# Performance work log

Measured on AMD Instinct MI355X. Metric: run time of the kernel, lower is better.

The kernel has to match this reference:

```python
import jax, jax.numpy as jnp
import numpy as np

B, N, T, F = 16, 512, 24, 64


def setup_inputs() -> dict:
    key = jax.random.key(0)
    k1, k2, k3, k4 = jax.random.split(key, 4)
    ori_flow = jax.random.normal(k1, (B, N, T, F), dtype=jnp.float32)
    uncer = jax.random.normal(k2, (B, N, T, F), dtype=jnp.float32)
    spatial_embedding = jax.random.normal(k3, (N, F), dtype=jnp.float32)
    # nn.Linear(channels, channels, bias=False): y = x @ W.T, W: (out, in)
    W1 = jax.random.normal(k4, (F, F), dtype=jnp.float32) * (1.0 / np.sqrt(F))
    return {"ori_flow": ori_flow, "uncer": uncer,
            "spatial_embedding": spatial_embedding, "W1": W1}


def reference(ori_flow, uncer, spatial_embedding, W1):
    b, n, t, f = ori_flow.shape
    # (B, N, T, f) -> (B*T, N, f)
    x = ori_flow.transpose(0, 2, 1, 3).reshape(-1, n, f)
    u = uncer.transpose(0, 2, 1, 3).reshape(-1, n, f)
    # spatial embedding is identical across batch and time after expand/permute
    emb = jnp.broadcast_to(spatial_embedding, (b * t, n, f))
    h = jnp.concatenate([x, emb], axis=-1)            # (B*T, N, 2f)
    rel = jax.nn.relu(jnp.einsum('bnf,bmf->bnm', h, h))  # (B*T, N, N)
    rel = jax.nn.softmax(rel, axis=-1)                # dropout p=0 -> identity
    # sharing_paras=True: both branches use linear1 (no bias)
    of = jax.nn.relu(jnp.einsum('bnm,bmf->bnf', rel, x) @ W1.T)
    uf = jax.nn.relu(jnp.einsum('bnm,bmf->bnf', rel, u) @ W1.T)
    of = of.reshape(b, t, n, f).transpose(0, 2, 1, 3)  # (B, N, T, f)
    uf = uf.reshape(b, t, n, f).transpose(0, 2, 1, 3)
    return of, uf
```

## Files before the change

### kernel.cpp

```cpp
#include <hip/hip_runtime.h>
#include <hip/hip_bf16.h>

#define BB 16
#define NN 512
#define TT 24
#define FF 64
#define OUT_OFF ((size_t)BB*NN*TT*FF)

#define AIS 136
#define XTS 72
#define XTSZ 4672

typedef __attribute__((ext_vector_type(8))) short v8s;
typedef __attribute__((ext_vector_type(16))) float v16f;

union U16x8 { uint4 v; unsigned short s[8]; };

__device__ inline v16f mfma32(v8s a, v8s b, v16f c) {
    return __builtin_amdgcn_mfma_f32_32x32x16_bf16(a, b, c, 0, 0, 0);
}

__device__ inline unsigned int fbits(float x) {
    union { float f; unsigned int u; } c; c.f = x; return c.u;
}
__device__ inline float ibits(unsigned int u) {
    union { float f; unsigned int u; } c; c.u = u; return c.f;
}
__device__ inline unsigned short f2bf_r(float x) {
    return (unsigned short)((fbits(x) + 0x8000u) >> 16);
}
__device__ inline void split8(const float* f, U16x8& H, U16x8& L) {
    #pragma unroll
    for (int k = 0; k < 8; ++k) {
        unsigned int u  = fbits(f[k]);
        unsigned int hr = (u + 0x8000u) & 0xffff0000u;
        H.s[k] = (unsigned short)(hr >> 16);
        float lo = f[k] - ibits(hr);
        L.s[k] = (unsigned short)((fbits(lo) + 0x8000u) >> 16);
    }
}
__device__ inline void cvt8h(const float* f, U16x8& H) {
    #pragma unroll
    for (int k = 0; k < 8; ++k) H.s[k] = f2bf_r(f[k]);
}

__device__ inline unsigned int pkbf(float a, float b) {
    unsigned int r;
    asm("v_cvt_pk_bf16_f32 %0, %1, %2" : "=v"(r) : "v"(a), "v"(b));
    return r;
}

__device__ inline v8s pfrag(const float* cr, int c) {
    unsigned int a0 = pkbf(cr[8*c+0], cr[8*c+1]);
    unsigned int a1 = pkbf(cr[8*c+2], cr[8*c+3]);
    unsigned int b0 = pkbf(cr[8*c+4], cr[8*c+5]);
    unsigned int b1 = pkbf(cr[8*c+6], cr[8*c+7]);
    asm("v_permlane32_swap_b32 %0, %1" : "+v"(a0), "+v"(b0));
    asm("v_permlane32_swap_b32 %0, %1" : "+v"(a1), "+v"(b1));
    union { v8s v; unsigned int u[4]; } P;
    P.u[0] = a0; P.u[1] = a1; P.u[2] = b0; P.u[3] = b1;
    return P.v;
}

__global__ __launch_bounds__(256, 2)
void spag_kernel(const float* __restrict__ ori, const float* __restrict__ unc,
                 const float* __restrict__ emb, const float* __restrict__ W1,
                 float* __restrict__ out)
{
    __shared__ __align__(16) unsigned short SH[2*64*AIS + 2*XTSZ];
    unsigned short* AjH = SH;
    unsigned short* AjL = SH + 64*AIS;
    unsigned short* XT  = SH + 2*64*AIS;
    unsigned short* UT  = XT + XTSZ;

    const int tid  = threadIdx.x;
    const int xcd  = blockIdx.x & 7;
    const int slot = blockIdx.x >> 3;
    const int bt   = xcd * 48 + (slot >> 2);
    const int it   = slot & 3;
    const int b    = bt / TT, t = bt % TT;
    const int i0   = it * 128;

    const int lane = tid & 63;
    const int w    = tid >> 6;
    const int m    = lane & 31;
    const int hi   = lane >> 5;

    const int pj  = tid >> 3;
    const int f0  = (tid & 7) * 8;
    const int jme = 2 * pj;

    float pa0[8], pa1[8], pu0[8], pu1[8];
    {
        const size_t r0 = ((size_t)((b*NN + jme)*TT + t))*FF + f0;
        const size_t r1 = r0 + (size_t)TT*FF;
        *(float4*)&pa0[0] = *(const float4*)(ori + r0);
        *(float4*)&pa0[4] = *(const float4*)(ori + r0 + 4);
        *(float4*)&pa1[0] = *(const float4*)(ori + r1);
        *(float4*)&pa1[4] = *(const float4*)(ori + r1 + 4);
        *(float4*)&pu0[0] = *(const float4*)(unc + r0);
        *(float4*)&pu0[4] = *(const float4*)(unc + r0 + 4);
        *(float4*)&pu1[0] = *(const float4*)(unc + r1);
        *(float4*)&pu1[4] = *(const float4*)(unc + r1 + 4);
    }

    v8s bH[8], bL[8];
    #pragma unroll
    for (int p = 0; p < 2; ++p) {
        {
            const int sr = tid >> 2, fc = (tid & 3) * 16;
            const float* xb = ori + ((size_t)((b*NN + i0 + p*64 + sr)*TT + t))*FF + fc;
            const float* eb = emb + (size_t)(i0 + p*64 + sr)*FF + fc;
            float tf[8]; U16x8 H, L;
            #pragma unroll
            for (int h = 0; h < 2; ++h) {
                *(float4*)&tf[0] = ((const float4*)xb)[2*h];
                *(float4*)&tf[4] = ((const float4*)xb)[2*h+1];
                split8(tf, H, L);
                *(uint4*)&AjH[sr*AIS + fc + h*8] = H.v;
                *(uint4*)&AjL[sr*AIS + fc + h*8] = L.v;
                *(float4*)&tf[0] = ((const float4*)eb)[2*h];
                *(float4*)&tf[4] = ((const float4*)eb)[2*h+1];
                split8(tf, H, L);
                *(uint4*)&AjH[sr*AIS + 64 + fc + h*8] = H.v;
                *(uint4*)&AjL[sr*AIS + 64 + fc + h*8] = L.v;
            }
        }
        __syncthreads();
        if ((w >> 1) == p) {
            const int lr = (w & 1)*32 + m;
            #pragma unroll
            for (int kk = 0; kk < 8; ++kk) {
                bH[kk] = *(const v8s*)&AjH[lr*AIS + kk*16 + hi*8];
                bL[kk] = *(const v8s*)&AjL[lr*AIS + kk*16 + hi*8];
            }
        }
        __syncthreads();
    }

    v16f accX0 = (v16f)(0.0f), accX1 = (v16f)(0.0f);
    v16f accU0 = (v16f)(0.0f), accU1 = (v16f)(0.0f);
    float rs    = 0.0f;
    float m_run = 0.0f;

    for (int jt = 0; jt < 8; ++jt) {
        const int j0 = jt * 64;
        __syncthreads();

        {
            const int j = jme;
            U16x8 H0, L0, H1, L1;
            split8(pa0, H0, L0); split8(pa1, H1, L1);
            *(uint4*)&AjH[ j   *AIS + f0] = H0.v;
            *(uint4*)&AjH[(j+1)*AIS + f0] = H1.v;
            *(uint4*)&AjL[ j   *AIS + f0] = L0.v;
            *(uint4*)&AjL[(j+1)*AIS + f0] = L1.v;
            #pragma unroll
            for (int k = 0; k < 8; ++k) {
                int f = f0 + k;
                int off = f*XTS + (f>>4)*16 + j;
                *(unsigned int*)&XT[off] =
                    (unsigned int)H0.s[k] | ((unsigned int)H1.s[k] << 16);
            }
            #pragma unroll
            for (int k = 0; k < 8; ++k) {
                int f = f0 + k;
                int off = f*XTS + (f>>4)*16 + j;
                *(unsigned int*)&UT[off] =
                    (unsigned int)f2bf_r(pu0[k]) | ((unsigned int)f2bf_r(pu1[k]) << 16);
            }
            const float* e0 = emb + (size_t)(j0 + j)*FF + f0;
            float t0[8], t1[8];
            *(float4*)&t0[0] = *(const float4*)(e0);
            *(float4*)&t0[4] = *(const float4*)(e0 + 4);
            *(float4*)&t1[0] = *(const float4*)(e0 + FF);
            *(float4*)&t1[4] = *(const float4*)(e0 + FF + 4);
            split8(t0, H0, L0); split8(t1, H1, L1);
            *(uint4*)&AjH[ j   *AIS + 64 + f0] = H0.v;
            *(uint4*)&AjH[(j+1)*AIS + 64 + f0] = H1.v;
            *(uint4*)&AjL[ j   *AIS + 64 + f0] = L0.v;
            *(uint4*)&AjL[(j+1)*AIS + 64 + f0] = L1.v;
        }
        __syncthreads();

        if (jt < 7) {
            const size_t r0 = ((size_t)((b*NN + j0 + 64 + jme)*TT + t))*FF + f0;
            const size_t r1 = r0 + (size_t)TT*FF;
            *(float4*)&pa0[0] = *(const float4*)(ori + r0);
            *(float4*)&pa0[4] = *(const float4*)(ori + r0 + 4);
            *(float4*)&pa1[0] = *(const float4*)(ori + r1);
            *(float4*)&pa1[4] = *(const float4*)(ori + r1 + 4);
            *(float4*)&pu0[0] = *(const float4*)(unc + r0);
            *(float4*)&pu0[4] = *(const float4*)(unc + r0 + 4);
            *(float4*)&pu1[0] = *(const float4*)(unc + r1);
            *(float4*)&pu1[4] = *(const float4*)(unc + r1 + 4);
        }

        v16f C0 = (v16f)(0.0f), C1 = (v16f)(0.0f);
        #pragma unroll
        for (int kk = 0; kk < 8; ++kk) {
            const int fo = kk*16 + hi*8;
            v8s aH0 = *(const v8s*)&AjH[ m     *AIS + fo];
            v8s aL0 = *(const v8s*)&AjL[ m     *AIS + fo];
            v8s aH1 = *(const v8s*)&AjH[(32+m)*AIS + fo];
            v8s aL1 = *(const v8s*)&AjL[(32+m)*AIS + fo];
            C0 = mfma32(aH0, bH[kk], C0);
            C1 = mfma32(aH1, bH[kk], C1);
            C0 = mfma32(aH0, bL[kk], C0);
            C1 = mfma32(aH1, bL[kk], C1);
            C0 = mfma32(aL0, bH[kk], C0);
            C1 = mfma32(aL1, bH[kk], C1);
        }

        float mt = 0.0f;
        #pragma unroll
        for (int r = 0; r < 16; ++r) {
            float s0 = fmaxf(C0[r], 0.0f); C0[r] = s0;
            float s1 = fmaxf(C1[r], 0.0f); C1[r] = s1;
            mt = fmaxf(mt, fmaxf(s0, s1));
        }
        mt = fmaxf(mt, __shfl_xor(mt, 32));
        if (!__all(mt <= m_run + 8.0f)) {
            float m_new = fmaxf(m_run, mt);
            float al = __expf(m_run - m_new);
            rs *= al; m_run = m_new;
            #pragma unroll
            for (int r = 0; r < 16; ++r) {
                float a = __shfl(al, (r & 3) + 8*(r >> 2) + 4*hi);
                accX0[r] *= a; accX1[r] *= a;
                accU0[r] *= a; accU1[r] *= a;
            }
        }

        v8s P[4];
        {
            float cr[16];
            #pragma unroll
            for (int r = 0; r < 16; ++r) {
                float e = __expf(C0[r] - m_run);
                cr[r] = ibits((fbits(e) + 0x8000u) & 0xffff0000u);
                rs += cr[r];
            }
            P[0] = pfrag(cr, 0);
            P[1] = pfrag(cr, 1);
            #pragma unroll
            for (int r = 0; r < 16; ++r) {
                float e = __expf(C1[r] - m_run);
                cr[r] = ibits((fbits(e) + 0x8000u) & 0xffff0000u);
                rs += cr[r];
            }
            P[2] = pfrag(cr, 0);
            P[3] = pfrag(cr, 1);
        }

        #pragma unroll
        for (int kk = 0; kk < 4; ++kk) {
            const int fo = kk*16 + hi*8;
            v8s bx0 = *(const v8s*)&XT[ m     *XTS + (( m    )>>4)*16 + fo];
            v8s bu0 = *(const v8s*)&UT[ m     *XTS + (( m    )>>4)*16 + fo];
            v8s bx1 = *(const v8s*)&XT[(32+m)*XTS + (((32+m))>>4)*16 + fo];
            v8s bu1 = *(const v8s*)&UT[(32+m)*XTS + (((32+m))>>4)*16 + fo];
            accX0 = mfma32(P[kk], bx0, accX0);
            accX1 = mfma32(P[kk], bx1, accX1);
            accU0 = mfma32(P[kk], bu0, accU0);
            accU1 = mfma32(P[kk], bu1, accU1);
        }
    }

    __syncthreads();
    rs += __shfl_xor(rs, 32);
    float inv = 1.0f / rs;

    unsigned short* Ox = SH;
    unsigned short* Ou = SH + 128*XTS;
    unsigned short* Wt = SH + 256*XTS;

    #pragma unroll
    for (int r = 0; r < 16; ++r) {
        int il = (r & 3) + 8*(r >> 2) + 4*hi;
        float iv = __shfl(inv, il);
        int row = w*32 + il;
        Ox[row*XTS + m]      = f2bf_r(accX0[r] * iv);
        Ox[row*XTS + 32 + m] = f2bf_r(accX1[r] * iv);
        Ou[row*XTS + m]      = f2bf_r(accU0[r] * iv);
        Ou[row*XTS + 32 + m] = f2bf_r(accU1[r] * iv);
    }
    {
        const int sr = tid >> 2, fc = (tid & 3) * 16;
        const float* wb = W1 + sr*FF + fc;
        float tf[8]; U16x8 H;
        #pragma unroll
        for (int h = 0; h < 2; ++h) {
            *(float4*)&tf[0] = ((const float4*)wb)[2*h];
            *(float4*)&tf[4] = ((const float4*)wb)[2*h+1];
            cvt8h(tf, H);
            *(uint4*)&Wt[sr*XTS + fc + h*8] = H.v;
        }
    }
    __syncthreads();

    v8s ao[4], aq[4];
    #pragma unroll
    for (int kk = 0; kk < 4; ++kk) {
        const int fo = kk*16 + hi*8;
        ao[kk] = *(const v8s*)&Ox[(w*32 + m)*XTS + fo];
        aq[kk] = *(const v8s*)&Ou[(w*32 + m)*XTS + fo];
    }
    #pragma unroll
    for (int ot = 0; ot < 2; ++ot) {
        v16f ax = (v16f)(0.0f), au = (v16f)(0.0f);
        #pragma unroll
        for (int kk = 0; kk < 4; ++kk) {
            const int fo = kk*16 + hi*8;
            v8s bw = *(const v8s*)&Wt[(ot*32 + m)*XTS + fo];
            ax = mfma32(ao[kk], bw, ax);
            au = mfma32(aq[kk], bw, au);
        }
        #pragma unroll
        for (int r = 0; r < 16; ++r) {
            int il = (r & 3) + 8*(r >> 2) + 4*hi;
            int i = i0 + w*32 + il;
            int o = ot*32 + m;
            size_t idx = ((size_t)((b*NN + i)*TT + t))*FF + o;
            out[idx]           = fmaxf(ax[r], 0.0f);
            out[OUT_OFF + idx] = fmaxf(au[r], 0.0f);
        }
    }
}

extern "C" void kernel_launch(void* const* d_in, const int* in_sizes, int n_in,
                              void* d_out, int out_size, void* d_ws, size_t ws_size,
                              hipStream_t stream) {
    const float* ori = (const float*)d_in[0];
    const float* unc = (const float*)d_in[1];
    const float* emb = (const float*)d_in[2];
    const float* W1  = (const float*)d_in[3];
    float* out = (float*)d_out;

    spag_kernel<<<dim3(BB*TT*4), dim3(256), 0, stream>>>(ori, unc, emb, W1, out);
}
```

Measured before the change: 265.1 us.

## Split score MFMA accumulators into two chains and raise occupancy to 3 blocks

The score GEMM's MFMA chain is split into two independent accumulator pairs, one over even and one over odd k-steps, which are summed afterwards. This breaks the serial dependency between back-to-back MFMAs on the same accumulator. Launch bounds also change from 2 to 3 blocks per CU, which tightens the register budget. Together with the 32 extra accumulator VGPRs, that risks spills or a compiler cap on registers.

```diff
diff --git a/kernel.cpp b/kernel.cpp
--- a/kernel.cpp
+++ b/kernel.cpp
@@ -62,7 +62,7 @@
     return P.v;
 }
 
-__global__ __launch_bounds__(256, 2)
+__global__ __launch_bounds__(256, 3)
 void spag_kernel(const float* __restrict__ ori, const float* __restrict__ unc,
                  const float* __restrict__ emb, const float* __restrict__ W1,
                  float* __restrict__ out)
@@ -196,21 +196,36 @@
             *(float4*)&pu1[4] = *(const float4*)(unc + r1 + 4);
         }
 
-        v16f C0 = (v16f)(0.0f), C1 = (v16f)(0.0f);
-        #pragma unroll
-        for (int kk = 0; kk < 8; ++kk) {
-            const int fo = kk*16 + hi*8;
-            v8s aH0 = *(const v8s*)&AjH[ m     *AIS + fo];
-            v8s aL0 = *(const v8s*)&AjL[ m     *AIS + fo];
-            v8s aH1 = *(const v8s*)&AjH[(32+m)*AIS + fo];
-            v8s aL1 = *(const v8s*)&AjL[(32+m)*AIS + fo];
-            C0 = mfma32(aH0, bH[kk], C0);
-            C1 = mfma32(aH1, bH[kk], C1);
-            C0 = mfma32(aH0, bL[kk], C0);
-            C1 = mfma32(aH1, bL[kk], C1);
-            C0 = mfma32(aL0, bH[kk], C0);
-            C1 = mfma32(aL1, bH[kk], C1);
-        }
+        v16f C0a = (v16f)(0.0f), C0b = (v16f)(0.0f);
+        v16f C1a = (v16f)(0.0f), C1b = (v16f)(0.0f);
+        #pragma unroll
+        for (int kk = 0; kk < 8; kk += 2) {
+            const int fo0 = kk*16 + hi*8;
+            const int fo1 = (kk+1)*16 + hi*8;
+            v8s aH0a = *(const v8s*)&AjH[ m     *AIS + fo0];
+            v8s aL0a = *(const v8s*)&AjL[ m     *AIS + fo0];
+            v8s aH1a = *(const v8s*)&AjH[(32+m)*AIS + fo0];
+            v8s aL1a = *(const v8s*)&AjL[(32+m)*AIS + fo0];
+            v8s aH0b = *(const v8s*)&AjH[ m     *AIS + fo1];
+            v8s aL0b = *(const v8s*)&AjL[ m     *AIS + fo1];
+            v8s aH1b = *(const v8s*)&AjH[(32+m)*AIS + fo1];
+            v8s aL1b = *(const v8s*)&AjL[(32+m)*AIS + fo1];
+            C0a = mfma32(aH0a, bH[kk],   C0a);
+            C1a = mfma32(aH1a, bH[kk],   C1a);
+            C0b = mfma32(aH0b, bH[kk+1], C0b);
+            C1b = mfma32(aH1b, bH[kk+1], C1b);
+            C0a = mfma32(aH0a, bL[kk],   C0a);
+            C1a = mfma32(aH1a, bL[kk],   C1a);
+            C0b = mfma32(aH0b, bL[kk+1], C0b);
+            C1b = mfma32(aH1b, bL[kk+1], C1b);
+            C0a = mfma32(aL0a, bH[kk],   C0a);
+            C1a = mfma32(aL1a, bH[kk],   C1a);
+            C0b = mfma32(aL0b, bH[kk+1], C0b);
+            C1b = mfma32(aL1b, bH[kk+1], C1b);
+        }
+        v16f C0, C1;
+        #pragma unroll
+        for (int r = 0; r < 16; ++r) { C0[r] = C0a[r] + C0b[r]; C1[r] = C1a[r] + C1b[r]; }
 
         float mt = 0.0f;
         #pragma unroll
```

Result: slower. 474.2 us (+78.9%).

## Software-pipeline P·V MFMAs one tile behind with double-buffered X/U tiles

Applied to the files above, without the earlier changes.

Double-buffers the transposed X/U bf16 tiles in shared memory and defers each tile's P·V MFMAs to the next iteration, so they are issued alongside the next tile's QK MFMAs and softmax exponentials. A drain step after the loop handles the last tile. The change also moves the hi/lo bf16 split and the X/U transposed stores to the packed v_cvt_pk_bf16_f32 instruction. It no longer pre-rounds the softmax weights before summing them, so the row sum now uses unrounded values while the MFMA still sees bf16-rounded ones. Shared memory grows by two tiles, which may reduce the two-blocks-per-CU occupancy.

```diff
diff --git a/kernel.cpp b/kernel.cpp
--- a/kernel.cpp
+++ b/kernel.cpp
@@ -14,7 +14,7 @@
 typedef __attribute__((ext_vector_type(8))) short v8s;
 typedef __attribute__((ext_vector_type(16))) float v16f;
 
-union U16x8 { uint4 v; unsigned short s[8]; };
+union U16x8 { uint4 v; unsigned int u[4]; unsigned short s[8]; };
 
 __device__ inline v16f mfma32(v8s a, v8s b, v16f c) {
     return __builtin_amdgcn_mfma_f32_32x32x16_bf16(a, b, c, 0, 0, 0);
@@ -29,25 +29,24 @@
 __device__ inline unsigned short f2bf_r(float x) {
     return (unsigned short)((fbits(x) + 0x8000u) >> 16);
 }
-__device__ inline void split8(const float* f, U16x8& H, U16x8& L) {
-    #pragma unroll
-    for (int k = 0; k < 8; ++k) {
-        unsigned int u  = fbits(f[k]);
-        unsigned int hr = (u + 0x8000u) & 0xffff0000u;
-        H.s[k] = (unsigned short)(hr >> 16);
-        float lo = f[k] - ibits(hr);
-        L.s[k] = (unsigned short)((fbits(lo) + 0x8000u) >> 16);
-    }
-}
-__device__ inline void cvt8h(const float* f, U16x8& H) {
-    #pragma unroll
-    for (int k = 0; k < 8; ++k) H.s[k] = f2bf_r(f[k]);
-}
-
 __device__ inline unsigned int pkbf(float a, float b) {
     unsigned int r;
     asm("v_cvt_pk_bf16_f32 %0, %1, %2" : "=v"(r) : "v"(a), "v"(b));
     return r;
+}
+__device__ inline void split8(const float* f, U16x8& H, U16x8& L) {
+    #pragma unroll
+    for (int k = 0; k < 4; ++k) {
+        unsigned int hp = pkbf(f[2*k], f[2*k+1]);
+        float h0 = ibits(hp << 16);
+        float h1 = ibits(hp & 0xffff0000u);
+        L.u[k] = pkbf(f[2*k] - h0, f[2*k+1] - h1);
+        H.u[k] = hp;
+    }
+}
+__device__ inline void cvt8h(const float* f, U16x8& H) {
+    #pragma unroll
+    for (int k = 0; k < 8; ++k) H.s[k] = f2bf_r(f[k]);
 }
 
 __device__ inline v8s pfrag(const float* cr, int c) {
@@ -67,11 +66,10 @@
                  const float* __restrict__ emb, const float* __restrict__ W1,
                  float* __restrict__ out)
 {
-    __shared__ __align__(16) unsigned short SH[2*64*AIS + 2*XTSZ];
+    __shared__ __align__(16) unsigned short SH[2*64*AIS + 4*XTSZ];
     unsigned short* AjH = SH;
     unsigned short* AjL = SH + 64*AIS;
-    unsigned short* XT  = SH + 2*64*AIS;
-    unsigned short* UT  = XT + XTSZ;
+    unsigned short* XTb = SH + 2*64*AIS;
 
     const int tid  = threadIdx.x;
     const int xcd  = blockIdx.x & 7;
@@ -142,9 +140,12 @@
     v16f accU0 = (v16f)(0.0f), accU1 = (v16f)(0.0f);
     float rs    = 0.0f;
     float m_run = 0.0f;
+    v8s Pv[4];
 
     for (int jt = 0; jt < 8; ++jt) {
         const int j0 = jt * 64;
+        unsigned short* XT = XTb + (jt & 1)*2*XTSZ;
+        unsigned short* UT = XT + XTSZ;
         __syncthreads();
 
         {
@@ -159,15 +160,8 @@
             for (int k = 0; k < 8; ++k) {
                 int f = f0 + k;
                 int off = f*XTS + (f>>4)*16 + j;
-                *(unsigned int*)&XT[off] =
-                    (unsigned int)H0.s[k] | ((unsigned int)H1.s[k] << 16);
-            }
-            #pragma unroll
-            for (int k = 0; k < 8; ++k) {
-                int f = f0 + k;
-                int off = f*XTS + (f>>4)*16 + j;
-                *(unsigned int*)&UT[off] =
-                    (unsigned int)f2bf_r(pu0[k]) | ((unsigned int)f2bf_r(pu1[k]) << 16);
+                *(unsigned int*)&XT[off] = pkbf(pa0[k], pa1[k]);
+                *(unsigned int*)&UT[off] = pkbf(pu0[k], pu1[k]);
             }
             const float* e0 = emb + (size_t)(j0 + j)*FF + f0;
             float t0[8], t1[8];
@@ -194,6 +188,23 @@
             *(float4*)&pu0[4] = *(const float4*)(unc + r0 + 4);
             *(float4*)&pu1[0] = *(const float4*)(unc + r1);
             *(float4*)&pu1[4] = *(const float4*)(unc + r1 + 4);
+        }
+
+        if (jt > 0) {
+            unsigned short* XTp = XTb + ((jt & 1) ^ 1)*2*XTSZ;
+            unsigned short* UTp = XTp + XTSZ;
+            #pragma unroll
+            for (int kk = 0; kk < 4; ++kk) {
+                const int fo = kk*16 + hi*8;
+                v8s bx0 = *(const v8s*)&XTp[ m     *XTS + (( m    )>>4)*16 + fo];
+                v8s bu0 = *(const v8s*)&UTp[ m     *XTS + (( m    )>>4)*16 + fo];
+                v8s bx1 = *(const v8s*)&XTp[(32+m)*XTS + (((32+m))>>4)*16 + fo];
+                v8s bu1 = *(const v8s*)&UTp[(32+m)*XTS + (((32+m))>>4)*16 + fo];
+                accX0 = mfma32(Pv[kk], bx0, accX0);
+                accX1 = mfma32(Pv[kk], bx1, accX1);
+                accU0 = mfma32(Pv[kk], bu0, accU0);
+                accU1 = mfma32(Pv[kk], bu1, accU1);
+            }
         }
 
         v16f C0 = (v16f)(0.0f), C1 = (v16f)(0.0f);
@@ -232,38 +243,41 @@
             }
         }
 
-        v8s P[4];
         {
             float cr[16];
             #pragma unroll
             for (int r = 0; r < 16; ++r) {
                 float e = __expf(C0[r] - m_run);
-                cr[r] = ibits((fbits(e) + 0x8000u) & 0xffff0000u);
-                rs += cr[r];
-            }
-            P[0] = pfrag(cr, 0);
-            P[1] = pfrag(cr, 1);
+                cr[r] = e;
+                rs += e;
+            }
+            Pv[0] = pfrag(cr, 0);
+            Pv[1] = pfrag(cr, 1);
             #pragma unroll
             for (int r = 0; r < 16; ++r) {
                 float e = __expf(C1[r] - m_run);
-                cr[r] = ibits((fbits(e) + 0x8000u) & 0xffff0000u);
-                rs += cr[r];
-            }
-            P[2] = pfrag(cr, 0);
-            P[3] = pfrag(cr, 1);
-        }
-
+                cr[r] = e;
+                rs += e;
+            }
+            Pv[2] = pfrag(cr, 0);
+            Pv[3] = pfrag(cr, 1);
+        }
+    }
+
+    {
+        unsigned short* XTp = XTb + 2*XTSZ;
+        unsigned short* UTp = XTp + XTSZ;
         #pragma unroll
         for (int kk = 0; kk < 4; ++kk) {
             const int fo = kk*16 + hi*8;
-            v8s bx0 = *(const v8s*)&XT[ m     *XTS + (( m    )>>4)*16 + fo];
-            v8s bu0 = *(const v8s*)&UT[ m     *XTS + (( m    )>>4)*16 + fo];
-            v8s bx1 = *(const v8s*)&XT[(32+m)*XTS + (((32+m))>>4)*16 + fo];
-            v8s bu1 = *(const v8s*)&UT[(32+m)*XTS + (((32+m))>>4)*16 + fo];
-            accX0 = mfma32(P[kk], bx0, accX0);
-            accX1 = mfma32(P[kk], bx1, accX1);
-            accU0 = mfma32(P[kk], bu0, accU0);
-            accU1 = mfma32(P[kk], bu1, accU1);
+            v8s bx0 = *(const v8s*)&XTp[ m     *XTS + (( m    )>>4)*16 + fo];
+            v8s bu0 = *(const v8s*)&UTp[ m     *XTS + (( m    )>>4)*16 + fo];
+            v8s bx1 = *(const v8s*)&XTp[(32+m)*XTS + (((32+m))>>4)*16 + fo];
+            v8s bu1 = *(const v8s*)&UTp[(32+m)*XTS + (((32+m))>>4)*16 + fo];
+            accX0 = mfma32(Pv[kk], bx0, accX0);
+            accX1 = mfma32(Pv[kk], bx1, accX1);
+            accU0 = mfma32(Pv[kk], bu0, accU0);
+            accU1 = mfma32(Pv[kk], bu1, accU1);
         }
     }
 
```

Result: faster. 254.8 us (-3.9%).
